# Optimization experiments

Measured on AMD Instinct MI355X. Metric: run time of the kernel, lower is better.

## Reference

```python
import jax, jax.numpy as jnp
import numpy as np

B, N, D, H = 64, 1024, 128, 64  # batch, max nodes, feat dim, hidden dim


def setup_inputs() -> dict:
    key = jax.random.key(0)
    k1, k2, k3, k4, k5, k6 = jax.random.split(key, 6)
    node_feat = jax.random.normal(k1, (B, N, D), dtype=jnp.float32)
    Laplacian = jax.random.normal(k2, (B, N, N), dtype=jnp.float32) / np.sqrt(N)
    # +/-1 labels as in a binary-margin loss
    label = jnp.where(jax.random.uniform(k3, (B,)) > 0.5, 1.0, -1.0).astype(jnp.float32)
    # kaiming-uniform-like init: bound = 1/sqrt(fan_in)
    W1 = jax.random.uniform(k4, (D, H), minval=-1.0, maxval=1.0, dtype=jnp.float32) / np.sqrt(D)
    W2 = jax.random.uniform(k5, (D, H), minval=-1.0, maxval=1.0, dtype=jnp.float32) / np.sqrt(D)
    Wl = jax.random.uniform(k6, (H, 1), minval=-1.0, maxval=1.0, dtype=jnp.float32) / np.sqrt(H)
    return {"node_feat": node_feat, "Laplacian": Laplacian, "label": label,
            "W1": W1, "W2": W2, "Wl": Wl}


def reference(node_feat, Laplacian, label, W1, W2, Wl):
    # msg = L @ tanh(x)                      [B,N,D]
    msg = jnp.einsum('bnm,bmd->bnd', Laplacian, jnp.tanh(node_feat))
    # state = tanh(x W1 + tanh(msg) W2)      [B,N,H]
    state = jnp.tanh(node_feat @ W1 + jnp.tanh(msg) @ W2)
    # readout: state Wl -> [B,N,1], mean-pool over nodes, scale by 1/H
    s = state @ Wl                                        # [B,N,1]
    logit = (s.mean(axis=1) / H).reshape(-1)              # [B]
    # softplus-style loss: mean log(1 + exp(-logit * label))
    loss = jnp.log1p(jnp.exp(-logit * label)).mean()
    return loss
```

## Files before the change

kernel.cpp:

```cpp
#include <hip/hip_runtime.h>

#define NB 64
#define NN 1024
#define ND 128
#define NH 64

typedef __attribute__((ext_vector_type(4))) float f32x4;
typedef __attribute__((ext_vector_type(8))) __bf16 bf16x8;

__device__ __forceinline__ ushort f2bf(float f) {
  unsigned u = __float_as_uint(f);
  u += 0x7fffu + ((u >> 16) & 1u);
  return (ushort)(u >> 16);
}

__global__ __launch_bounds__(256) void prep_kernel(const float* __restrict__ x,
                                                   ushort* __restrict__ txt,
                                                   float* __restrict__ acc) {
  if (blockIdx.x == 0 && blockIdx.y == 0 && blockIdx.z == 0 && threadIdx.x < NB)
    acc[threadIdx.x] = 0.0f;
  __shared__ ushort tile[64][72];
  int b = blockIdx.z;
  int n0 = blockIdx.x * 64;
  int d0 = blockIdx.y * 64;
  int tid = threadIdx.x;
  int r = tid >> 2;
  int cseg = (tid & 3) * 16;
  const float* xp = x + ((size_t)b * NN + n0 + r) * ND + d0 + cseg;
  #pragma unroll
  for (int i = 0; i < 16; i += 4) {
    float4 v = *(const float4*)(xp + i);
    ushort4 w;
    w.x = f2bf(tanhf(v.x)); w.y = f2bf(tanhf(v.y));
    w.z = f2bf(tanhf(v.z)); w.w = f2bf(tanhf(v.w));
    *(ushort4*)&tile[r][cseg + i] = w;
  }
  __syncthreads();
  ushort* op = txt + ((size_t)b * ND + d0 + r) * NN + n0 + cseg;
  #pragma unroll
  for (int i = 0; i < 16; i += 4) {
    ushort4 w;
    w.x = tile[cseg + i + 0][r];
    w.y = tile[cseg + i + 1][r];
    w.z = tile[cseg + i + 2][r];
    w.w = tile[cseg + i + 3][r];
    *(ushort4*)(op + i) = w;
  }
}

__global__ __launch_bounds__(256) void msg_kernel(const float* __restrict__ L,
                                                  const ushort* __restrict__ txt,
                                                  ushort* __restrict__ tmsg) {
  __shared__ ushort As[64][72];
  __shared__ ushort Bs[128][72];
  int b = blockIdx.y;
  int brow = blockIdx.x * 64;
  int tid = threadIdx.x;
  int wave = tid >> 6, lane = tid & 63;
  int wm = (wave >> 1) * 32;
  int wn = (wave & 1) * 64;
  int l15 = lane & 15;
  int kof = (lane >> 4) * 8;
  const float*  Lp = L   + (size_t)b * NN * NN;
  const ushort* Bp = txt + (size_t)b * ND * NN;
  f32x4 acc[2][4] = {};
  int ar = tid >> 2, aseg = (tid & 3) * 16;
  int bd = tid >> 1, bseg = (tid & 1) * 32;
  for (int k0 = 0; k0 < NN; k0 += 64) {
    const float* ap = Lp + (size_t)(brow + ar) * NN + k0 + aseg;
    #pragma unroll
    for (int i = 0; i < 16; i += 4) {
      float4 v = *(const float4*)(ap + i);
      ushort4 w;
      w.x = f2bf(v.x); w.y = f2bf(v.y); w.z = f2bf(v.z); w.w = f2bf(v.w);
      *(ushort4*)&As[ar][aseg + i] = w;
    }
    const float4* bp = (const float4*)(Bp + (size_t)bd * NN + k0 + bseg);
    #pragma unroll
    for (int i = 0; i < 4; ++i)
      *(float4*)&Bs[bd][bseg + i * 8] = bp[i];
    __syncthreads();
    #pragma unroll
    for (int kk = 0; kk < 2; ++kk) {
      int kb = kk * 32 + kof;
      bf16x8 a0 = *(const bf16x8*)&As[wm + l15][kb];
      bf16x8 a1 = *(const bf16x8*)&As[wm + 16 + l15][kb];
      #pragma unroll
      for (int nt = 0; nt < 4; ++nt) {
        bf16x8 bb = *(const bf16x8*)&Bs[wn + nt * 16 + l15][kb];
        acc[0][nt] = __builtin_amdgcn_mfma_f32_16x16x32_bf16(a0, bb, acc[0][nt], 0, 0, 0);
        acc[1][nt] = __builtin_amdgcn_mfma_f32_16x16x32_bf16(a1, bb, acc[1][nt], 0, 0, 0);
      }
    }
    __syncthreads();
  }
  ushort* op = tmsg + (size_t)b * NN * ND;
  #pragma unroll
  for (int mt = 0; mt < 2; ++mt)
    #pragma unroll
    for (int nt = 0; nt < 4; ++nt)
      #pragma unroll
      for (int rr = 0; rr < 4; ++rr) {
        int row = brow + wm + mt * 16 + (lane >> 4) * 4 + rr;
        int col = wn + nt * 16 + l15;
        op[(size_t)row * ND + col] = f2bf(tanhf(acc[mt][nt][rr]));
      }
}

__global__ __launch_bounds__(256) void state_kernel(const float* __restrict__ x,
                                                    const ushort* __restrict__ tmsg,
                                                    const float* __restrict__ W1,
                                                    const float* __restrict__ W2,
                                                    const float* __restrict__ Wl,
                                                    float* __restrict__ acc) {
  __shared__ ushort W1t[64][136];
  __shared__ ushort W2t[64][136];
  __shared__ ushort Xs[64][136];
  __shared__ ushort Ts[64][136];
  __shared__ float Wls[64];
  int b = blockIdx.y;
  int n0 = blockIdx.x * 64;
  int tid = threadIdx.x;
  for (int i = tid; i < ND * NH; i += 256) {
    int d = i >> 6, h = i & 63;
    W1t[h][d] = f2bf(W1[i]);
    W2t[h][d] = f2bf(W2[i]);
  }
  if (tid < NH) Wls[tid] = Wl[tid];
  int r = tid >> 2, seg = (tid & 3) * 32;
  const float* xp = x + ((size_t)b * NN + n0 + r) * ND + seg;
  #pragma unroll
  for (int i = 0; i < 32; i += 4) {
    float4 v = *(const float4*)(xp + i);
    ushort4 w;
    w.x = f2bf(v.x); w.y = f2bf(v.y); w.z = f2bf(v.z); w.w = f2bf(v.w);
    *(ushort4*)&Xs[r][seg + i] = w;
  }
  const ushort* tp = tmsg + ((size_t)b * NN + n0 + r) * ND + seg;
  #pragma unroll
  for (int i = 0; i < 4; ++i)
    *(float4*)&Ts[r][seg + i * 8] = *(const float4*)(tp + i * 8);
  __syncthreads();
  int wave = tid >> 6, lane = tid & 63;
  int l15 = lane & 15, kof = (lane >> 4) * 8;
  int arow = wave * 16 + l15;
  f32x4 acc4[4] = {};
  #pragma unroll
  for (int kk = 0; kk < 4; ++kk) {
    int kb = kk * 32 + kof;
    bf16x8 ax = *(const bf16x8*)&Xs[arow][kb];
    bf16x8 at = *(const bf16x8*)&Ts[arow][kb];
    #pragma unroll
    for (int nt = 0; nt < 4; ++nt) {
      bf16x8 b1 = *(const bf16x8*)&W1t[nt * 16 + l15][kb];
      bf16x8 b2 = *(const bf16x8*)&W2t[nt * 16 + l15][kb];
      acc4[nt] = __builtin_amdgcn_mfma_f32_16x16x32_bf16(ax, b1, acc4[nt], 0, 0, 0);
      acc4[nt] = __builtin_amdgcn_mfma_f32_16x16x32_bf16(at, b2, acc4[nt], 0, 0, 0);
    }
  }
  float ssum = 0.0f;
  #pragma unroll
  for (int rr = 0; rr < 4; ++rr) {
    #pragma unroll
    for (int nt = 0; nt < 4; ++nt) {
      float st = tanhf(acc4[nt][rr]);
      ssum += st * Wls[nt * 16 + l15];
    }
  }
  #pragma unroll
  for (int off = 32; off >= 1; off >>= 1)
    ssum += __shfl_xor(ssum, off);
  if (lane == 0) atomicAdd(&acc[b], ssum);
}

__global__ void final_kernel(const float* __restrict__ acc,
                             const float* __restrict__ label,
                             float* __restrict__ out) {
  int t = threadIdx.x;
  float v = 0.0f;
  if (t < NB) {
    float logit = acc[t] * (1.0f / ((float)NN * (float)NH));
    float z = -logit * label[t];
    v = log1pf(expf(z));
  }
  #pragma unroll
  for (int off = 32; off >= 1; off >>= 1)
    v += __shfl_xor(v, off);
  if (t == 0) out[0] = v * (1.0f / (float)NB);
}

extern "C" void kernel_launch(void* const* d_in, const int* in_sizes, int n_in,
                              void* d_out, int out_size, void* d_ws, size_t ws_size,
                              hipStream_t stream) {
  const float* x     = (const float*)d_in[0];
  const float* L     = (const float*)d_in[1];
  const float* label = (const float*)d_in[2];
  const float* W1    = (const float*)d_in[3];
  const float* W2    = (const float*)d_in[4];
  const float* Wl    = (const float*)d_in[5];
  float* out = (float*)d_out;

  char* ws = (char*)d_ws;
  ushort* txt  = (ushort*)ws;
  ushort* tmsg = (ushort*)(ws + (size_t)16777216);
  float*  acc  = (float*)(ws + (size_t)33554432);

  prep_kernel<<<dim3(NN / 64, ND / 64, NB), 256, 0, stream>>>(x, txt, acc);
  msg_kernel<<<dim3(NN / 64, NB), 256, 0, stream>>>(L, txt, tmsg);
  state_kernel<<<dim3(NN / 64, NB), 256, 0, stream>>>(x, tmsg, W1, W2, Wl, acc);
  final_kernel<<<1, 64, 0, stream>>>(acc, label, out);
}
```

Measured before the change: 457.5 us.

## Load msg GEMM tiles directly into LDS via global_load_lds, convert A at read

The msg GEMM now stages the fp32 Laplacian tile and the bf16 tanh(x) tile straight from global memory into shared memory with the direct-to-LDS load builtin, skipping the register round trip. The fp32-to-bf16 conversion of the Laplacian moves from the store phase to the fragment-read phase, using the native bf16 cast instead of manual rounding. This frees VGPRs and load/store instructions, but doubles A-tile LDS footprint, removes padding (possible bank conflicts), and repeats the conversion work per wave that shares rows.

After: 456.2 us. About the same (-0.3%).

```diff
diff --git a/kernel.cpp b/kernel.cpp
--- a/kernel.cpp
+++ b/kernel.cpp
@@ -13,6 +13,11 @@
   u += 0x7fffu + ((u >> 16) & 1u);
   return (ushort)(u >> 16);
 }
+
+#define GLOAD16(g, l)                                                          \
+  __builtin_amdgcn_global_load_lds(                                            \
+      (const __attribute__((address_space(1))) void*)(g),                      \
+      (__attribute__((address_space(3))) void*)(l), 16, 0, 0)
 
 __global__ __launch_bounds__(256) void prep_kernel(const float* __restrict__ x,
                                                    ushort* __restrict__ txt,
@@ -51,49 +56,60 @@
 __global__ __launch_bounds__(256) void msg_kernel(const float* __restrict__ L,
                                                   const ushort* __restrict__ txt,
                                                   ushort* __restrict__ tmsg) {
-  __shared__ ushort As[64][72];
-  __shared__ ushort Bs[128][72];
+  __shared__ float  As[64 * 64];
+  __shared__ ushort Bs[128 * 64];
   int b = blockIdx.y;
   int brow = blockIdx.x * 64;
   int tid = threadIdx.x;
   int wave = tid >> 6, lane = tid & 63;
+  int l15 = lane & 15;
+  int kof = (lane >> 4) * 8;
   int wm = (wave >> 1) * 32;
   int wn = (wave & 1) * 64;
-  int l15 = lane & 15;
-  int kof = (lane >> 4) * 8;
-  const float*  Lp = L   + (size_t)b * NN * NN;
-  const ushort* Bp = txt + (size_t)b * ND * NN;
+
+  const char* Lb = (const char*)(L + (size_t)b * NN * NN + (size_t)brow * NN);
+  const char* Tb = (const char*)(txt + (size_t)b * ND * NN);
+
+  const char* aG = Lb + (size_t)(4 * (wave * 4) + (lane >> 4)) * (NN * 4) + l15 * 16;
+  const char* bG = Tb + (size_t)(8 * (wave * 4) + (lane >> 3)) * (NN * 2) + (lane & 7) * 16;
+  char* aL = (char*)As + (wave * 4) * 1024;
+  char* bL = (char*)Bs + (wave * 4) * 1024;
+
   f32x4 acc[2][4] = {};
-  int ar = tid >> 2, aseg = (tid & 3) * 16;
-  int bd = tid >> 1, bseg = (tid & 1) * 32;
+
   for (int k0 = 0; k0 < NN; k0 += 64) {
-    const float* ap = Lp + (size_t)(brow + ar) * NN + k0 + aseg;
-    #pragma unroll
-    for (int i = 0; i < 16; i += 4) {
-      float4 v = *(const float4*)(ap + i);
-      ushort4 w;
-      w.x = f2bf(v.x); w.y = f2bf(v.y); w.z = f2bf(v.z); w.w = f2bf(v.w);
-      *(ushort4*)&As[ar][aseg + i] = w;
-    }
-    const float4* bp = (const float4*)(Bp + (size_t)bd * NN + k0 + bseg);
     #pragma unroll
     for (int i = 0; i < 4; ++i)
-      *(float4*)&Bs[bd][bseg + i * 8] = bp[i];
+      GLOAD16(aG + (size_t)i * 4 * (NN * 4) + (size_t)k0 * 4, aL + i * 1024);
+    #pragma unroll
+    for (int i = 0; i < 4; ++i)
+      GLOAD16(bG + (size_t)i * 8 * (NN * 2) + (size_t)k0 * 2, bL + i * 1024);
     __syncthreads();
     #pragma unroll
     for (int kk = 0; kk < 2; ++kk) {
       int kb = kk * 32 + kof;
-      bf16x8 a0 = *(const bf16x8*)&As[wm + l15][kb];
-      bf16x8 a1 = *(const bf16x8*)&As[wm + 16 + l15][kb];
+      bf16x8 av[2];
+      #pragma unroll
+      for (int mt = 0; mt < 2; ++mt) {
+        const f32x4* ap = (const f32x4*)(As + (wm + mt * 16 + l15) * 64 + kb);
+        f32x4 lo = ap[0], hi = ap[1];
+        bf16x8 a;
+        a[0] = (__bf16)lo[0]; a[1] = (__bf16)lo[1];
+        a[2] = (__bf16)lo[2]; a[3] = (__bf16)lo[3];
+        a[4] = (__bf16)hi[0]; a[5] = (__bf16)hi[1];
+        a[6] = (__bf16)hi[2]; a[7] = (__bf16)hi[3];
+        av[mt] = a;
+      }
       #pragma unroll
       for (int nt = 0; nt < 4; ++nt) {
-        bf16x8 bb = *(const bf16x8*)&Bs[wn + nt * 16 + l15][kb];
-        acc[0][nt] = __builtin_amdgcn_mfma_f32_16x16x32_bf16(a0, bb, acc[0][nt], 0, 0, 0);
-        acc[1][nt] = __builtin_amdgcn_mfma_f32_16x16x32_bf16(a1, bb, acc[1][nt], 0, 0, 0);
+        bf16x8 bb = *(const bf16x8*)(Bs + (wn + nt * 16 + l15) * 64 + kb);
+        acc[0][nt] = __builtin_amdgcn_mfma_f32_16x16x32_bf16(av[0], bb, acc[0][nt], 0, 0, 0);
+        acc[1][nt] = __builtin_amdgcn_mfma_f32_16x16x32_bf16(av[1], bb, acc[1][nt], 0, 0, 0);
       }
     }
     __syncthreads();
   }
+
   ushort* op = tmsg + (size_t)b * NN * ND;
   #pragma unroll
   for (int mt = 0; mt < 2; ++mt)
```
